# Kernel tuning notes

Hardware: AMD Instinct MI355X
Metric: run time of the kernel (lower is better)

The kernel has to match this reference:

```python
import jax, jax.numpy as jnp
import numpy as np

N = 30000   # nodes
E = 480000  # edges (avg degree 16)
D = 256     # feat_dim == dim
H = 8       # heads
C = 32      # out channels per head (D // H, concat=True)
NEG = 0.2   # leaky-relu negative slope (args.alpha)
L = 2       # num_layers
NENC = 2 * L  # two GATv2 encoders (source/target direction) per layer


def setup_inputs() -> dict:
    key = jax.random.key(0)
    ks = jax.random.split(key, 10)
    s = jax.random.normal(ks[0], (N, D), dtype=jnp.float32)
    t = jax.random.normal(ks[1], (N, D), dtype=jnp.float32)
    edge_index = jax.random.randint(ks[2], (2, E), 0, N, dtype=jnp.int32)
    scale = 0.05
    Wl = jax.random.normal(ks[3], (NENC, D, H * C), dtype=jnp.float32) * scale
    bl = jnp.zeros((NENC, H * C), dtype=jnp.float32)
    Wr = jax.random.normal(ks[4], (NENC, D, H * C), dtype=jnp.float32) * scale
    br = jnp.zeros((NENC, H * C), dtype=jnp.float32)
    att = jax.random.normal(ks[5], (NENC, H, C), dtype=jnp.float32) * scale
    bias = jnp.zeros((NENC, H * C), dtype=jnp.float32)
    return {"s": s, "t": t, "Wl": Wl, "bl": bl, "Wr": Wr, "br": br,
            "att": att, "bias": bias, "edge_index": edge_index}


def _gatv2(x_src, x_dst, src, dst, Wl, bl, Wr, br, att, bias):
    """PyG GATv2Conv on bipartite input ((x_src, x_dst), edge_index).
    Messages flow src->dst, softmax-normalized over incoming edges of dst."""
    hl = (x_src @ Wl + bl).reshape(N, H, C)  # lin_l(source)
    hr = (x_dst @ Wr + br).reshape(N, H, C)  # lin_r(target)
    xe = hl[src] + hr[dst]                    # [E,H,C]
    e = jnp.where(xe > 0, xe, NEG * xe)       # leaky_relu
    logits = jnp.einsum('ehc,hc->eh', e, att)  # [E,H]
    m = jax.ops.segment_max(logits, dst, num_segments=N)
    m = jnp.where(jnp.isfinite(m), m, jnp.zeros_like(m))  # empty segments
    p = jnp.exp(logits - m[dst])
    denom = jax.ops.segment_sum(p, dst, num_segments=N)
    alpha = p / (denom[dst] + 1e-16)          # scatter-softmax weights [E,H]
    out = jax.ops.segment_sum(alpha[:, :, None] * hl[src], dst, num_segments=N)
    return out.reshape(N, H * C) + bias       # concat heads + bias


def reference(s, t, Wl, bl, Wr, br, att, bias, edge_index):
    src, dst = edge_index[0], edge_index[1]
    x_s, x_t = s, t
    for l in range(L):
        i, j = 2 * l, 2 * l + 1
        # source_encoder((s, t), edges): aggregate s-messages at t-nodes
        sh = _gatv2(x_s, x_t, src, dst, Wl[i], bl[i], Wr[i], br[i], att[i], bias[i])
        # target_encoder((t, s), flipped edges)
        th = _gatv2(x_t, x_s, dst, src, Wl[j], bl[j], Wr[j], br[j], att[j], bias[j])
        if l < L - 1:  # last layer activation is identity
            sh = jax.nn.relu(sh)
            th = jax.nn.relu(th)
        x_s, x_t = sh, th
    return x_s, x_t
```

## Files before the change

kernel.cpp:

```cpp
#include <hip/hip_runtime.h>
#include <hip/hip_bf16.h>

#define NNODES 30000
#define NEDGES 480000
#define HC 256
#define NEG_SLOPE 0.2f
#define NPART 8
#define EPP 60000
#define PN (NPART * NNODES)
#define SCAN_CHUNK 1024
#define NCHUNK2 235
#define NCHUNKM 30
#define CPP 235
#define NFE 7680000

typedef _Float16 half8 __attribute__((ext_vector_type(8)));
typedef _Float16 h4v __attribute__((ext_vector_type(4)));
typedef _Float16 h2 __attribute__((ext_vector_type(2)));
typedef float floatx4 __attribute__((ext_vector_type(4)));


__global__ void prep_kernel(const float* __restrict__ Wl, const float* __restrict__ Wr,
                            _Float16* __restrict__ WtL, _Float16* __restrict__ WtR,
                            const int* __restrict__ ei, int* __restrict__ deg_dst,
                            int* __restrict__ deg_src) {
    __shared__ float sh[32][33];
    int b = blockIdx.x;
    if (b < 512) {
        int e = b >> 6;
        int r0 = ((b >> 3) & 7) * 32, c0 = (b & 7) * 32;
        const float* W = (e < 4) ? Wl + (size_t)e * 65536 : Wr + (size_t)(e - 4) * 65536;
        _Float16* Wt = (e < 4) ? WtL + (size_t)e * 65536 : WtR + (size_t)(e - 4) * 65536;
        int x = threadIdx.x & 31, y = threadIdx.x >> 5;
#pragma unroll
        for (int j = 0; j < 4; j++) {
            int r = y + j * 8;
            sh[r][x] = W[(size_t)(r0 + r) * 256 + c0 + x];
        }
        __syncthreads();
#pragma unroll
        for (int j = 0; j < 4; j++) {
            int nn = y + j * 8;
            Wt[(size_t)(c0 + nn) * 256 + r0 + x] = (_Float16)sh[x][nn];
        }
    } else {
        b -= 512;
        int p = b & 7, c = b >> 3;
        int idx = c * 256 + threadIdx.x;
        if (idx >= EPP) return;
        int e = p * EPP + idx;
        int s = ei[e];
        int d = ei[NEDGES + e];
        atomicAdd(&deg_dst[p * NNODES + d], 1);
        atomicAdd(&deg_src[p * NNODES + s], 1);
    }
}

__global__ void mdeg_kernel(const int* __restrict__ deg_dst, const int* __restrict__ deg_src,
                            int* __restrict__ mdeg_dst, int* __restrict__ mdeg_src) {
    const int* deg = blockIdx.y ? deg_src : deg_dst;
    int* mdeg = blockIdx.y ? mdeg_src : mdeg_dst;
    int n = blockIdx.x * blockDim.x + threadIdx.x;
    if (n >= NNODES) return;
    int s = 0;
#pragma unroll
    for (int p = 0; p < NPART; p++) s += deg[p * NNODES + n];
    mdeg[n] = s;
}


__global__ void scanA_kernel(const int* __restrict__ deg_dst, const int* __restrict__ deg_src,
                             const int* __restrict__ mdeg_dst, const int* __restrict__ mdeg_src,
                             int* __restrict__ cur_dst, int* __restrict__ cur_src,
                             int* __restrict__ mrp_dst, int* __restrict__ mrp_src,
                             int* __restrict__ bsum) {
    __shared__ int sh[SCAN_CHUNK];
    const int y = blockIdx.y;
    const int nelem = (y < 2) ? PN : NNODES;
    if (blockIdx.x * SCAN_CHUNK >= nelem) return;
    const int* in = (y == 0) ? deg_dst : (y == 1) ? deg_src : (y == 2) ? mdeg_dst : mdeg_src;
    int t = threadIdx.x;
    int gid = blockIdx.x * SCAN_CHUNK + t;
    int v = (gid < nelem) ? in[gid] : 0;
    sh[t] = v;
    __syncthreads();
    for (int off = 1; off < SCAN_CHUNK; off <<= 1) {
        int u = (t >= off) ? sh[t - off] : 0;
        __syncthreads();
        sh[t] += u;
        __syncthreads();
    }
    if (gid < nelem) {
        if (y < 2) {
            int* cur = (y == 0) ? cur_dst : cur_src;
            cur[gid] = sh[t] - v;
        } else {
            int* mrp = (y == 2) ? mrp_dst : mrp_src;
            mrp[gid + 1] = sh[t];
        }
    }
    if (t == SCAN_CHUNK - 1) bsum[y * 256 + blockIdx.x] = sh[t];
}

__global__ void scan2_kernel(int* __restrict__ bsum) {
    int t = threadIdx.x;
    if (t < 4) {
        int cnt = (t < 2) ? NCHUNK2 : NCHUNKM;
        int run = 0;
        for (int i = 0; i < cnt; i++) {
            int v = bsum[t * 256 + i];
            bsum[t * 256 + i] = run;
            run += v;
        }
    }
}

__global__ void scanB_kernel(int* __restrict__ cur_dst, int* __restrict__ cur_src,
                             int* __restrict__ mrp_dst, int* __restrict__ mrp_src,
                             const int* __restrict__ bsum) {
    const int y = blockIdx.y;
    const int nelem = (y < 2) ? PN : NNODES;
    if (blockIdx.x * SCAN_CHUNK >= nelem) return;
    int t = threadIdx.x;
    int gid = blockIdx.x * SCAN_CHUNK + t;
    int base = bsum[y * 256 + blockIdx.x];
    if (gid < nelem) {
        if (y < 2) {
            ((y == 0) ? cur_dst : cur_src)[gid] += base;
        } else {
            ((y == 2) ? mrp_dst : mrp_src)[gid + 1] += base;
        }
    }
    if (gid == 0 && y >= 2) ((y == 2) ? mrp_dst : mrp_src)[0] = 0;
}

__global__ void fill_kernel(const int* __restrict__ ei, int* __restrict__ cur_dst,
                            int* __restrict__ cur_src, unsigned short* __restrict__ col_dst,
                            unsigned short* __restrict__ col_src) {
    int p = blockIdx.x & 7, c = blockIdx.x >> 3;
    int idx = c * 256 + threadIdx.x;
    if (idx >= EPP) return;
    int e = p * EPP + idx;
    int s = ei[e];
    int d = ei[NEDGES + e];
    int p0 = atomicAdd(&cur_dst[p * NNODES + d], 1);
    col_dst[p0] = (unsigned short)s;
    int p1 = atomicAdd(&cur_src[p * NNODES + s], 1);
    col_src[p1] = (unsigned short)d;
}

__global__ void merge_kernel(const int* __restrict__ deg_dst, const int* __restrict__ deg_src,
                             const int* __restrict__ cur_dst, const int* __restrict__ cur_src,
                             const int* __restrict__ mrp_dst, const int* __restrict__ mrp_src,
                             const unsigned short* __restrict__ col_dst,
                             const unsigned short* __restrict__ col_src,
                             unsigned short* __restrict__ mcol_dst,
                             unsigned short* __restrict__ mcol_src) {
    const int z = blockIdx.y;
    const int* deg = z ? deg_src : deg_dst;
    const int* cur = z ? cur_src : cur_dst;
    const int* mrp = z ? mrp_src : mrp_dst;
    const unsigned short* col = z ? col_src : col_dst;
    unsigned short* mcol = z ? mcol_src : mcol_dst;
    int n = blockIdx.x * blockDim.x + threadIdx.x;
    if (n >= NNODES) return;
    int w = mrp[n];
#pragma unroll
    for (int p = 0; p < NPART; p++) {
        int e = cur[p * NNODES + n];
        int d = deg[p * NNODES + n];
        for (int k = e - d; k < e; k++) mcol[w++] = col[k];
    }
}


__device__ inline half8 ldA8(const _Float16* p) { return *(const half8*)p; }
__device__ inline half8 ldA8(const float* p) {
    float4 a = *(const float4*)p;
    float4 b = *(const float4*)(p + 4);
    half8 r = {(_Float16)a.x, (_Float16)a.y, (_Float16)a.z, (_Float16)a.w,
               (_Float16)b.x, (_Float16)b.y, (_Float16)b.z, (_Float16)b.w};
    return r;
}

#define EPI_STRIDE 264

template <typename AT>
__global__ void __launch_bounds__(256)
gemm_f16(const AT* __restrict__ xs, const AT* __restrict__ xt,
         const _Float16* __restrict__ WtL, const _Float16* __restrict__ WtR,
         const float* __restrict__ bl, const float* __restrict__ br,
         _Float16* __restrict__ hbase, int e0) {
    const int y = blockIdx.y;
    const int e = e0 + (y >> 1);
    const AT* A = (y == 0 || y == 3) ? xs : xt;
    const bool left = (y & 1) == 0;
    const _Float16* Wt = (left ? WtL : WtR) + (size_t)e * 65536;
    const float* bvec = (left ? bl : br) + (size_t)e * HC;
    _Float16* C = hbase + (size_t)y * NFE;

    __shared__ __align__(16) _Float16 sh[10240];
    _Float16* As = sh;
    _Float16* Bs = sh + 2048;

    const int t = threadIdx.x;
    const int lane = t & 63, w = t >> 6;
    const int m0 = blockIdx.x * 64;
    const int rl = lane & 15, ch = lane >> 4;
    const int ar = t >> 2, ac = t & 3;

    floatx4 acc[4][4] = {};

    half8 av = {};
    {
        int gr = m0 + ar;
        if (gr < NNODES) av = ldA8(A + (size_t)gr * 256 + ac * 8);
    }
    half8 bv[4];
#pragma unroll
    for (int j = 0; j < 4; j++)
        bv[j] = *(const half8*)(Wt + (size_t)(ar + j * 64) * 256 + ac * 8);

    for (int k0 = 0; k0 < 256; k0 += 32) {
        __syncthreads();
        *(half8*)(As + ar * 32 + (ac ^ ((ar >> 1) & 3)) * 8) = av;
#pragma unroll
        for (int j = 0; j < 4; j++) {
            int n = ar + j * 64;
            *(half8*)(Bs + n * 32 + (ac ^ ((n >> 1) & 3)) * 8) = bv[j];
        }
        __syncthreads();

        if (k0 + 32 < 256) {
            int gr = m0 + ar;
            if (gr < NNODES) av = ldA8(A + (size_t)gr * 256 + (k0 + 32) + ac * 8);
#pragma unroll
            for (int j = 0; j < 4; j++)
                bv[j] = *(const half8*)(Wt + (size_t)(ar + j * 64) * 256 + (k0 + 32) + ac * 8);
        }

        half8 a[4], b[4];
#pragma unroll
        for (int fm = 0; fm < 4; fm++) {
            int r = fm * 16 + rl;
            a[fm] = *(const half8*)(As + r * 32 + (ch ^ ((r >> 1) & 3)) * 8);
        }
#pragma unroll
        for (int fn = 0; fn < 4; fn++) {
            int n = w * 64 + fn * 16 + rl;
            b[fn] = *(const half8*)(Bs + n * 32 + (ch ^ ((n >> 1) & 3)) * 8);
        }
#pragma unroll
        for (int fm = 0; fm < 4; fm++)
#pragma unroll
            for (int fn = 0; fn < 4; fn++)
                acc[fm][fn] = __builtin_amdgcn_mfma_f32_16x16x32_f16(a[fm], b[fn], acc[fm][fn], 0, 0, 0);
    }

    float bb[4];
#pragma unroll
    for (int fn = 0; fn < 4; fn++) bb[fn] = bvec[w * 64 + fn * 16 + rl];

#pragma unroll
    for (int hh = 0; hh < 2; hh++) {
        __syncthreads();
#pragma unroll
        for (int f2 = 0; f2 < 2; f2++) {
            int fm = hh * 2 + f2;
#pragma unroll
            for (int fn = 0; fn < 4; fn++) {
                int colb = w * 64 + fn * 16 + rl;
#pragma unroll
                for (int j = 0; j < 4; j++) {
                    int lr = f2 * 16 + ch * 4 + j;
                    sh[lr * EPI_STRIDE + colb] = (_Float16)(acc[fm][fn][j] + bb[fn]);
                }
            }
        }
        __syncthreads();
        int lr = t >> 3;
        int cseg = (t & 7) * 32;
        int gr = m0 + hh * 32 + lr;
        if (gr < NNODES) {
#pragma unroll
            for (int q = 0; q < 4; q++)
                *(half8*)(C + (size_t)gr * 256 + cseg + q * 8) =
                    *(const half8*)(sh + lr * EPI_STRIDE + cseg + q * 8);
        }
    }
}


__device__ __forceinline__ void edge_body(half8 hv, half8 hrv, const float* att8,
                                          float* acc, float& denom, bool valid) {
    const h2 negv = {(_Float16)NEG_SLOPE, (_Float16)NEG_SLOPE};
    const h2* hvp = (const h2*)&hv;
    const h2* hrp = (const h2*)&hrv;
    float v = 0.f;
#pragma unroll
    for (int k = 0; k < 4; k++) {
        h2 x = hvp[k] + hrp[k];
        h2 lk = __builtin_elementwise_max(x, x * negv);
        v = fmaf((float)lk[0], att8[2 * k], v);
        v = fmaf((float)lk[1], att8[2 * k + 1], v);
    }
    v += __shfl_xor(v, 1);
    v += __shfl_xor(v, 2);
    float pe = __expf(v);
    if (!valid) pe = 0.f;
    denom += pe;
#pragma unroll
    for (int k = 0; k < 8; k++) acc[k] = fmaf((float)hv[k], pe, acc[k]);
}

__device__ inline void store8(float* p, const float* o) {
    *(float4*)p = make_float4(o[0], o[1], o[2], o[3]);
    *(float4*)(p + 4) = make_float4(o[4], o[5], o[6], o[7]);
}
__device__ inline void store8(_Float16* p, const float* o) {
    half8 h = {(_Float16)o[0], (_Float16)o[1], (_Float16)o[2], (_Float16)o[3],
               (_Float16)o[4], (_Float16)o[5], (_Float16)o[6], (_Float16)o[7]};
    *(half8*)p = h;
}

template <typename OT>
__global__ void __launch_bounds__(256)
agg_kernel(const _Float16* __restrict__ hbase,
           const int* __restrict__ mrp_dst, const unsigned short* __restrict__ mcol_dst,
           const int* __restrict__ mrp_src, const unsigned short* __restrict__ mcol_src,
           const float* __restrict__ att, const float* __restrict__ bias,
           OT* __restrict__ out0, OT* __restrict__ out1, int e0, int do_relu) {
    const int z = blockIdx.y;
    const _Float16* hl = hbase + (size_t)z * 2 * NFE;
    const _Float16* hr = hl + NFE;
    const int* mrp = z ? mrp_src : mrp_dst;
    const unsigned short* mcol = z ? mcol_src : mcol_dst;
    const float* attz = att + (size_t)(e0 + z) * HC;
    const float* biasz = bias + (size_t)(e0 + z) * HC;
    OT* out = z ? out1 : out0;

    int wave = threadIdx.x >> 6;
    int lane = threadIdx.x & 63;
    int n = blockIdx.x * 4 + wave;
    if (n >= NNODES) return;
    int h = lane >> 5;
    int cl = lane & 31;
    int c8 = cl << 3;

    const _Float16* hlc = hl + c8;
    half8 hrv = *(const half8*)(hr + (size_t)n * HC + c8);
    float att8[8];
    *(float4*)(att8) = *(const float4*)(attz + c8);
    *(float4*)(att8 + 4) = *(const float4*)(attz + c8 + 4);

    float acc[8] = {};
    float denom = 0.f;
    int beg = mrp[n], end = mrp[n + 1];

    int i = beg;
    for (; i + 8 <= end; i += 8) {
        int s0 = (int)mcol[i + h];
        int s1 = (int)mcol[i + 2 + h];
        int s2 = (int)mcol[i + 4 + h];
        int s3 = (int)mcol[i + 6 + h];
        half8 hv0 = *(const half8*)(hlc + ((size_t)s0 << 8));
        half8 hv1 = *(const half8*)(hlc + ((size_t)s1 << 8));
        half8 hv2 = *(const half8*)(hlc + ((size_t)s2 << 8));
        half8 hv3 = *(const half8*)(hlc + ((size_t)s3 << 8));
        edge_body(hv0, hrv, att8, acc, denom, true);
        edge_body(hv1, hrv, att8, acc, denom, true);
        edge_body(hv2, hrv, att8, acc, denom, true);
        edge_body(hv3, hrv, att8, acc, denom, true);
    }
    for (; i + 2 <= end; i += 2) {
        int s0 = (int)mcol[i + h];
        half8 hv0 = *(const half8*)(hlc + ((size_t)s0 << 8));
        edge_body(hv0, hrv, att8, acc, denom, true);
    }
    if (i < end) {
        bool valid = (h == 0);
        int s0 = (int)mcol[i];
        half8 hv0 = *(const half8*)(hlc + ((size_t)s0 << 8));
        edge_body(hv0, hrv, att8, acc, denom, valid);
    }

#pragma unroll
    for (int k = 0; k < 8; k++) acc[k] += __shfl_xor(acc[k], 32);
    denom += __shfl_xor(denom, 32);

    if (lane < 32) {
        float inv = 1.f / (denom + 1e-16f);
        float o[8];
        float b8[8];
        *(float4*)(b8) = *(const float4*)(biasz + c8);
        *(float4*)(b8 + 4) = *(const float4*)(biasz + c8 + 4);
#pragma unroll
        for (int k = 0; k < 8; k++) {
            o[k] = acc[k] * inv + b8[k];
            if (do_relu) o[k] = fmaxf(o[k], 0.f);
        }
        store8(out + (size_t)n * HC + c8, o);
    }
}


extern "C" void kernel_launch(void* const* d_in, const int* in_sizes, int n_in,
                              void* d_out, int out_size, void* d_ws, size_t ws_size,
                              hipStream_t stream) {
    const float* s = (const float*)d_in[0];
    const float* t = (const float*)d_in[1];
    const float* Wl = (const float*)d_in[2];
    const float* bl = (const float*)d_in[3];
    const float* Wr = (const float*)d_in[4];
    const float* br = (const float*)d_in[5];
    const float* att = (const float*)d_in[6];
    const float* bias = (const float*)d_in[7];
    const int* ei = (const int*)d_in[8];
    float* out = (float*)d_out;

    const size_t NF = (size_t)NFE;

    _Float16* os16 = (_Float16*)d_ws;
    _Float16* ot16 = os16 + NF;
    _Float16* hbase = ot16 + NF;
    _Float16* WtL = hbase + 4 * NF;
    _Float16* WtR = WtL + 4 * 65536;
    int* deg_dst = (int*)(WtR + 4 * 65536);
    int* deg_src = deg_dst + PN;
    int* cur_dst = deg_src + PN;
    int* cur_src = cur_dst + PN;
    int* mdeg_dst = cur_src + PN;
    int* mdeg_src = mdeg_dst + NNODES;
    int* mrp_dst = mdeg_src + NNODES;
    int* mrp_src = mrp_dst + (NNODES + 1);
    int* bsum = mrp_src + (NNODES + 1);
    unsigned short* col_dst = (unsigned short*)(bsum + 1024);
    unsigned short* col_src = col_dst + NEDGES;
    unsigned short* mcol_dst = col_src + NEDGES;
    unsigned short* mcol_src = mcol_dst + NEDGES;

    hipMemsetAsync(deg_dst, 0, 2 * PN * sizeof(int), stream);
    prep_kernel<<<512 + NPART * CPP, 256, 0, stream>>>(Wl, Wr, WtL, WtR, ei, deg_dst, deg_src);
    mdeg_kernel<<<dim3(118, 2), 256, 0, stream>>>(deg_dst, deg_src, mdeg_dst, mdeg_src);
    {
        dim3 g(NCHUNK2, 4);
        scanA_kernel<<<g, SCAN_CHUNK, 0, stream>>>(deg_dst, deg_src, mdeg_dst, mdeg_src,
                                                   cur_dst, cur_src, mrp_dst, mrp_src, bsum);
        scan2_kernel<<<1, 64, 0, stream>>>(bsum);
        scanB_kernel<<<g, SCAN_CHUNK, 0, stream>>>(cur_dst, cur_src, mrp_dst, mrp_src, bsum);
    }
    fill_kernel<<<NPART * CPP, 256, 0, stream>>>(ei, cur_dst, cur_src, col_dst, col_src);
    merge_kernel<<<dim3(118, 2), 256, 0, stream>>>(deg_dst, deg_src, cur_dst, cur_src,
                                                   mrp_dst, mrp_src, col_dst, col_src,
                                                   mcol_dst, mcol_src);

    dim3 ggemm((NNODES + 63) / 64, 4);
    dim3 gagg((NNODES + 3) / 4, 2);

    gemm_f16<float><<<ggemm, 256, 0, stream>>>(s, t, WtL, WtR, bl, br, hbase, 0);
    agg_kernel<_Float16><<<gagg, 256, 0, stream>>>(hbase, mrp_dst, mcol_dst, mrp_src, mcol_src,
                                                   att, bias, os16, ot16, 0, 1);
    gemm_f16<_Float16><<<ggemm, 256, 0, stream>>>(os16, ot16, WtL, WtR, bl, br, hbase, 2);
    agg_kernel<float><<<gagg, 256, 0, stream>>>(hbase, mrp_dst, mcol_dst, mrp_src, mcol_src,
                                                att, bias, out, out + NF, 2, 0);
}
```

Measured before the change: 377.6 us.

## Fuse degree merge into scan, widen GEMM K-tile, use fdot2 and nontemporal stores

Folds the per-node degree sum into the scan kernel, which removes one kernel launch and an intermediate buffer. The GEMM K-step grows from 32 to 64, doubling shared memory and changing the swizzle, so there are half as many sync/load rounds. The attention dot product now uses fp16 fdot2 with attention weights converted to half, which can lose precision. The aggregation loop unroll drops from 8 to 4 with a unified tail, and outputs and the hr load become nontemporal.

After: 444.6 us. 1.18x slower.

```diff
diff --git a/kernel.cpp b/kernel.cpp
--- a/kernel.cpp
+++ b/kernel.cpp
@@ -56,21 +56,8 @@
     }
 }
 
-__global__ void mdeg_kernel(const int* __restrict__ deg_dst, const int* __restrict__ deg_src,
-                            int* __restrict__ mdeg_dst, int* __restrict__ mdeg_src) {
-    const int* deg = blockIdx.y ? deg_src : deg_dst;
-    int* mdeg = blockIdx.y ? mdeg_src : mdeg_dst;
-    int n = blockIdx.x * blockDim.x + threadIdx.x;
-    if (n >= NNODES) return;
-    int s = 0;
-#pragma unroll
-    for (int p = 0; p < NPART; p++) s += deg[p * NNODES + n];
-    mdeg[n] = s;
-}
-
 
 __global__ void scanA_kernel(const int* __restrict__ deg_dst, const int* __restrict__ deg_src,
-                             const int* __restrict__ mdeg_dst, const int* __restrict__ mdeg_src,
                              int* __restrict__ cur_dst, int* __restrict__ cur_src,
                              int* __restrict__ mrp_dst, int* __restrict__ mrp_src,
                              int* __restrict__ bsum) {
@@ -78,10 +65,18 @@
     const int y = blockIdx.y;
     const int nelem = (y < 2) ? PN : NNODES;
     if (blockIdx.x * SCAN_CHUNK >= nelem) return;
-    const int* in = (y == 0) ? deg_dst : (y == 1) ? deg_src : (y == 2) ? mdeg_dst : mdeg_src;
     int t = threadIdx.x;
     int gid = blockIdx.x * SCAN_CHUNK + t;
-    int v = (gid < nelem) ? in[gid] : 0;
+    int v = 0;
+    if (gid < nelem) {
+        if (y == 0) v = deg_dst[gid];
+        else if (y == 1) v = deg_src[gid];
+        else {
+            const int* deg = (y == 2) ? deg_dst : deg_src;
+#pragma unroll
+            for (int p = 0; p < NPART; p++) v += deg[p * NNODES + gid];
+        }
+    }
     sh[t] = v;
     __syncthreads();
     for (int off = 1; off < SCAN_CHUNK; off <<= 1) {
@@ -92,11 +87,9 @@
     }
     if (gid < nelem) {
         if (y < 2) {
-            int* cur = (y == 0) ? cur_dst : cur_src;
-            cur[gid] = sh[t] - v;
+            ((y == 0) ? cur_dst : cur_src)[gid] = sh[t] - v;
         } else {
-            int* mrp = (y == 2) ? mrp_dst : mrp_src;
-            mrp[gid + 1] = sh[t];
+            ((y == 2) ? mrp_dst : mrp_src)[gid + 1] = sh[t];
         }
     }
     if (t == SCAN_CHUNK - 1) bsum[y * 256 + blockIdx.x] = sh[t];
@@ -199,9 +192,9 @@
     const float* bvec = (left ? bl : br) + (size_t)e * HC;
     _Float16* C = hbase + (size_t)y * NFE;
 
-    __shared__ __align__(16) _Float16 sh[10240];
+    __shared__ __align__(16) _Float16 sh[20480];
     _Float16* As = sh;
-    _Float16* Bs = sh + 2048;
+    _Float16* Bs = sh + 4096;
 
     const int t = threadIdx.x;
     const int lane = t & 63, w = t >> 6;
@@ -211,50 +204,73 @@
 
     floatx4 acc[4][4] = {};
 
-    half8 av = {};
+    half8 av[2] = {};
+    half8 bv[8];
     {
         int gr = m0 + ar;
-        if (gr < NNODES) av = ldA8(A + (size_t)gr * 256 + ac * 8);
-    }
-    half8 bv[4];
-#pragma unroll
-    for (int j = 0; j < 4; j++)
-        bv[j] = *(const half8*)(Wt + (size_t)(ar + j * 64) * 256 + ac * 8);
-
-    for (int k0 = 0; k0 < 256; k0 += 32) {
-        __syncthreads();
-        *(half8*)(As + ar * 32 + (ac ^ ((ar >> 1) & 3)) * 8) = av;
-#pragma unroll
-        for (int j = 0; j < 4; j++) {
-            int n = ar + j * 64;
-            *(half8*)(Bs + n * 32 + (ac ^ ((n >> 1) & 3)) * 8) = bv[j];
-        }
-        __syncthreads();
-
-        if (k0 + 32 < 256) {
+        if (gr < NNODES) {
+            av[0] = ldA8(A + (size_t)gr * 256 + ac * 16);
+            av[1] = ldA8(A + (size_t)gr * 256 + ac * 16 + 8);
+        }
+    }
+#pragma unroll
+    for (int j = 0; j < 4; j++) {
+        const _Float16* bp = Wt + (size_t)(ar + j * 64) * 256 + ac * 16;
+        bv[2 * j] = *(const half8*)bp;
+        bv[2 * j + 1] = *(const half8*)(bp + 8);
+    }
+
+    for (int k0 = 0; k0 < 256; k0 += 64) {
+        __syncthreads();
+        {
+            int c0 = ac * 2;
+            int m = ar & 7;
+            *(half8*)(As + ar * 64 + (c0 ^ m) * 8) = av[0];
+            *(half8*)(As + ar * 64 + ((c0 + 1) ^ m) * 8) = av[1];
+#pragma unroll
+            for (int j = 0; j < 4; j++) {
+                int n = ar + j * 64;
+                *(half8*)(Bs + n * 64 + (c0 ^ m) * 8) = bv[2 * j];
+                *(half8*)(Bs + n * 64 + ((c0 + 1) ^ m) * 8) = bv[2 * j + 1];
+            }
+        }
+        __syncthreads();
+
+        if (k0 + 64 < 256) {
             int gr = m0 + ar;
-            if (gr < NNODES) av = ldA8(A + (size_t)gr * 256 + (k0 + 32) + ac * 8);
-#pragma unroll
-            for (int j = 0; j < 4; j++)
-                bv[j] = *(const half8*)(Wt + (size_t)(ar + j * 64) * 256 + (k0 + 32) + ac * 8);
-        }
-
-        half8 a[4], b[4];
-#pragma unroll
-        for (int fm = 0; fm < 4; fm++) {
-            int r = fm * 16 + rl;
-            a[fm] = *(const half8*)(As + r * 32 + (ch ^ ((r >> 1) & 3)) * 8);
-        }
-#pragma unroll
-        for (int fn = 0; fn < 4; fn++) {
-            int n = w * 64 + fn * 16 + rl;
-            b[fn] = *(const half8*)(Bs + n * 32 + (ch ^ ((n >> 1) & 3)) * 8);
-        }
-#pragma unroll
-        for (int fm = 0; fm < 4; fm++)
-#pragma unroll
-            for (int fn = 0; fn < 4; fn++)
-                acc[fm][fn] = __builtin_amdgcn_mfma_f32_16x16x32_f16(a[fm], b[fn], acc[fm][fn], 0, 0, 0);
+            if (gr < NNODES) {
+                av[0] = ldA8(A + (size_t)gr * 256 + (k0 + 64) + ac * 16);
+                av[1] = ldA8(A + (size_t)gr * 256 + (k0 + 64) + ac * 16 + 8);
+            }
+#pragma unroll
+            for (int j = 0; j < 4; j++) {
+                const _Float16* bp = Wt + (size_t)(ar + j * 64) * 256 + (k0 + 64) + ac * 16;
+                bv[2 * j] = *(const half8*)bp;
+                bv[2 * j + 1] = *(const half8*)(bp + 8);
+            }
+        }
+
+#pragma unroll
+        for (int kk = 0; kk < 2; kk++) {
+            half8 a[4], b[4];
+#pragma unroll
+            for (int fm = 0; fm < 4; fm++) {
+                int r = fm * 16 + rl;
+                int c = kk * 4 + ch;
+                a[fm] = *(const half8*)(As + r * 64 + (c ^ (r & 7)) * 8);
+            }
+#pragma unroll
+            for (int fn = 0; fn < 4; fn++) {
+                int n = w * 64 + fn * 16 + rl;
+                int c = kk * 4 + ch;
+                b[fn] = *(const half8*)(Bs + n * 64 + (c ^ (n & 7)) * 8);
+            }
+#pragma unroll
+            for (int fm = 0; fm < 4; fm++)
+#pragma unroll
+                for (int fn = 0; fn < 4; fn++)
+                    acc[fm][fn] = __builtin_amdgcn_mfma_f32_16x16x32_f16(a[fm], b[fn], acc[fm][fn], 0, 0, 0);
+        }
     }
 
     float bb[4];
@@ -284,14 +300,14 @@
         if (gr < NNODES) {
 #pragma unroll
             for (int q = 0; q < 4; q++)
-                *(half8*)(C + (size_t)gr * 256 + cseg + q * 8) =
-                    *(const half8*)(sh + lr * EPI_STRIDE + cseg + q * 8);
-        }
-    }
-}
-
-
-__device__ __forceinline__ void edge_body(half8 hv, half8 hrv, const float* att8,
+                __builtin_nontemporal_store(*(const half8*)(sh + lr * EPI_STRIDE + cseg + q * 8),
+                                            (half8*)(C + (size_t)gr * 256 + cseg + q * 8));
+        }
+    }
+}
+
+
+__device__ __forceinline__ void edge_body(half8 hv, half8 hrv, const h2* att2,
                                           float* acc, float& denom, bool valid) {
     const h2 negv = {(_Float16)NEG_SLOPE, (_Float16)NEG_SLOPE};
     const h2* hvp = (const h2*)&hv;
@@ -301,8 +317,7 @@
     for (int k = 0; k < 4; k++) {
         h2 x = hvp[k] + hrp[k];
         h2 lk = __builtin_elementwise_max(x, x * negv);
-        v = fmaf((float)lk[0], att8[2 * k], v);
-        v = fmaf((float)lk[1], att8[2 * k + 1], v);
+        v = __builtin_amdgcn_fdot2(lk, att2[k], v, false);
     }
     v += __shfl_xor(v, 1);
     v += __shfl_xor(v, 2);
@@ -314,13 +329,15 @@
 }
 
 __device__ inline void store8(float* p, const float* o) {
-    *(float4*)p = make_float4(o[0], o[1], o[2], o[3]);
-    *(float4*)(p + 4) = make_float4(o[4], o[5], o[6], o[7]);
+    floatx4 v0 = {o[0], o[1], o[2], o[3]};
+    floatx4 v1 = {o[4], o[5], o[6], o[7]};
+    __builtin_nontemporal_store(v0, (floatx4*)p);
+    __builtin_nontemporal_store(v1, (floatx4*)(p + 4));
 }
 __device__ inline void store8(_Float16* p, const float* o) {
     half8 h = {(_Float16)o[0], (_Float16)o[1], (_Float16)o[2], (_Float16)o[3],
                (_Float16)o[4], (_Float16)o[5], (_Float16)o[6], (_Float16)o[7]};
-    *(half8*)p = h;
+    __builtin_nontemporal_store(h, (half8*)p);
 }
 
 template <typename OT>
@@ -348,40 +365,33 @@
     int c8 = cl << 3;
 
     const _Float16* hlc = hl + c8;
-    half8 hrv = *(const half8*)(hr + (size_t)n * HC + c8);
-    float att8[8];
-    *(float4*)(att8) = *(const float4*)(attz + c8);
-    *(float4*)(att8 + 4) = *(const float4*)(attz + c8 + 4);
+    half8 hrv = __builtin_nontemporal_load((const half8*)(hr + (size_t)n * HC + c8));
+    float attf[8];
+    *(float4*)(attf) = *(const float4*)(attz + c8);
+    *(float4*)(attf + 4) = *(const float4*)(attz + c8 + 4);
+    h2 att2[4];
+#pragma unroll
+    for (int k = 0; k < 4; k++) att2[k] = h2{(_Float16)attf[2 * k], (_Float16)attf[2 * k + 1]};
 
     float acc[8] = {};
     float denom = 0.f;
     int beg = mrp[n], end = mrp[n + 1];
 
     int i = beg;
-    for (; i + 8 <= end; i += 8) {
+    for (; i + 4 <= end; i += 4) {
         int s0 = (int)mcol[i + h];
         int s1 = (int)mcol[i + 2 + h];
-        int s2 = (int)mcol[i + 4 + h];
-        int s3 = (int)mcol[i + 6 + h];
         half8 hv0 = *(const half8*)(hlc + ((size_t)s0 << 8));
         half8 hv1 = *(const half8*)(hlc + ((size_t)s1 << 8));
-        half8 hv2 = *(const half8*)(hlc + ((size_t)s2 << 8));
-        half8 hv3 = *(const half8*)(hlc + ((size_t)s3 << 8));
-        edge_body(hv0, hrv, att8, acc, denom, true);
-        edge_body(hv1, hrv, att8, acc, denom, true);
-        edge_body(hv2, hrv, att8, acc, denom, true);
-        edge_body(hv3, hrv, att8, acc, denom, true);
-    }
-    for (; i + 2 <= end; i += 2) {
-        int s0 = (int)mcol[i + h];
+        edge_body(hv0, hrv, att2, acc, denom, true);
+        edge_body(hv1, hrv, att2, acc, denom, true);
+    }
+    for (; i < end; i += 2) {
+        int ei = i + h;
+        bool valid = ei < end;
+        int s0 = (int)mcol[valid ? ei : end - 1];
         half8 hv0 = *(const half8*)(hlc + ((size_t)s0 << 8));
-        edge_body(hv0, hrv, att8, acc, denom, true);
-    }
-    if (i < end) {
-        bool valid = (h == 0);
-        int s0 = (int)mcol[i];
-        half8 hv0 = *(const half8*)(hlc + ((size_t)s0 << 8));
-        edge_body(hv0, hrv, att8, acc, denom, valid);
+        edge_body(hv0, hrv, att2, acc, denom, valid);
     }
 
 #pragma unroll
@@ -429,9 +439,7 @@
     int* deg_src = deg_dst + PN;
     int* cur_dst = deg_src + PN;
     int* cur_src = cur_dst + PN;
-    int* mdeg_dst = cur_src + PN;
-    int* mdeg_src = mdeg_dst + NNODES;
-    int* mrp_dst = mdeg_src + NNODES;
+    int* mrp_dst = cur_src + PN;
     int* mrp_src = mrp_dst + (NNODES + 1);
     int* bsum = mrp_src + (NNODES + 1);
     unsigned short* col_dst = (unsigned short*)(bsum + 1024);
@@ -441,11 +449,10 @@
 
     hipMemsetAsync(deg_dst, 0, 2 * PN * sizeof(int), stream);
     prep_kernel<<<512 + NPART * CPP, 256, 0, stream>>>(Wl, Wr, WtL, WtR, ei, deg_dst, deg_src);
-    mdeg_kernel<<<dim3(118, 2), 256, 0, stream>>>(deg_dst, deg_src, mdeg_dst, mdeg_src);
     {
         dim3 g(NCHUNK2, 4);
-        scanA_kernel<<<g, SCAN_CHUNK, 0, stream>>>(deg_dst, deg_src, mdeg_dst, mdeg_src,
-                                                   cur_dst, cur_src, mrp_dst, mrp_src, bsum);
+        scanA_kernel<<<g, SCAN_CHUNK, 0, stream>>>(deg_dst, deg_src, cur_dst, cur_src,
+                                                   mrp_dst, mrp_src, bsum);
         scan2_kernel<<<1, 64, 0, stream>>>(bsum);
         scanB_kernel<<<g, SCAN_CHUNK, 0, stream>>>(cur_dst, cur_src, mrp_dst, mrp_src, bsum);
     }
```
